# Performance work log

Measured on AMD Instinct MI355X. Metric: run time of the kernel, lower is better.

The kernel has to match this reference:

```python
import jax, jax.numpy as jnp
import numpy as np

N, D, H, B = 8192, 1024, 100, 32  # pairs, key dim, MLP hidden, batch_size


def setup_inputs() -> dict:
    key = jax.random.key(0)
    ks = jax.random.split(key, 6)
    q = jax.random.normal(ks[0], (N, D), jnp.float32)
    x = jax.random.normal(ks[1], (N, D), jnp.float32)
    b = jax.random.randint(ks[2], (N,), 0, B, dtype=jnp.int32)
    y = jax.random.randint(ks[3], (N,), 0, 2, dtype=jnp.int32)
    # Encoder params: Linear(2D -> H), ReLU, Linear(H -> 1)
    W1 = jax.random.normal(ks[4], (2 * D, H), jnp.float32) * (1.0 / np.sqrt(2 * D))
    b1 = jnp.zeros((H,), jnp.float32)
    W2 = jax.random.normal(ks[5], (H, 1), jnp.float32) * (1.0 / np.sqrt(H))
    b2 = jnp.zeros((1,), jnp.float32)
    return {"b": b, "q": q, "x": x, "y": y, "W1": W1, "b1": b1, "W2": W2, "b2": b2}


def reference(b, q, x, y, W1, b1, W2, b2):
    # Encoder: score per (query, key) pair
    inp = jnp.concatenate([q, x], axis=1)              # (N, 2D)
    h = jax.nn.relu(inp @ W1 + b1)                     # (N, H)
    s = (h @ W2 + b2)[:, 0]                            # (N,)

    n = s.shape[0]
    r = jnp.arange(n)
    yb = y.astype(bool)
    # pair mask: same batch element, differing labels, upper triangle
    m = (b[:, None] == b[None, :]) \
        & (yb[:, None] ^ yb[None, :]) \
        & (r[:, None] < r[None, :])                    # (N, N) bool

    d = s[:, None] - s[None, :]                        # (N, N) score diffs (logits)
    z = y.astype(jnp.float32)[:, None]                 # row label broadcast as target
    # stable BCE-with-logits, masked mean (== BCEWithLogitsLoss over selected pairs)
    bce = jnp.maximum(d, 0.0) - d * z + jnp.log1p(jnp.exp(-jnp.abs(d)))
    mf = m.astype(jnp.float32)
    loss = jnp.sum(bce * mf) / jnp.sum(mf)
    return loss
```

## Files before the change

### kernel.cpp

```cpp
#include <hip/hip_runtime.h>
#include <math.h>
#include <stdint.h>

#define NN 8192
#define DD 1024
#define KT 2048
#define HH 100
#define HP 128
#define LCAP 512
#define NB 32
#define NCH 16

typedef short bf16x8 __attribute__((ext_vector_type(8)));
typedef short bf16x4 __attribute__((ext_vector_type(4)));
typedef float f32x4 __attribute__((ext_vector_type(4)));

__device__ __forceinline__ short f2bf(float f) {
    uint32_t u = __builtin_bit_cast(uint32_t, f);
    u += 0x7FFF + ((u >> 16) & 1);
    return (short)(u >> 16);
}

__global__ __launch_bounds__(256) void prep_w1p(const float* __restrict__ W1,
                                                short* __restrict__ w1p,
                                                int* __restrict__ cnt1,
                                                int* __restrict__ cnt0)
{
    __shared__ float ld[32][104];
    const int t  = threadIdx.x;
    if (blockIdx.x == 0 && t < 64) {
        if (t < 32) cnt1[t] = 0; else cnt0[t - 32] = 0;
    }
    const int k0 = blockIdx.x * 32;
    for (int i = t; i < 32 * HH; i += 256) {
        const int kk = i / HH, cc = i - kk * HH;
        ld[kk][cc] = W1[(size_t)(k0 + kk) * HH + cc];
    }
    __syncthreads();
    for (int idx = t; idx < 512; idx += 256) {
        const int tt = idx >> 6, l = idx & 63;
        const int lr = l & 15, lg = l >> 4;
        const int col = tt * 16 + lr;
        bf16x8 r;
#pragma unroll
        for (int j = 0; j < 8; ++j)
            r[j] = (col < HH) ? f2bf(ld[lg * 8 + j][col]) : (short)0;
        *(bf16x8*)(w1p + ((size_t)(blockIdx.x * 8 + tt) * 64 + l) * 8) = r;
    }
}

__global__ __launch_bounds__(512) void encoder_mfma(
    const float* __restrict__ q, const float* __restrict__ x,
    const short* __restrict__ w1p,
    const float* __restrict__ b1, const float* __restrict__ W2,
    const float* __restrict__ b2,
    const int* __restrict__ bidx, const int* __restrict__ y,
    float* __restrict__ sp, float* __restrict__ sn,
    int* __restrict__ cnt1, int* __restrict__ cnt0)
{
    __shared__ short As[2][16][NCH][64];
    __shared__ float hsum[16][HP + 4];
    __shared__ float fold[4][16];
    const int t    = threadIdx.x;
    const int w    = t >> 6;
    const int half = w >> 2;
    const int wc   = w & 3;
    const int l    = t & 63;
    const int lr   = l & 15;
    const int lg   = l >> 4;
    const int r0   = blockIdx.x * 16;

    const int ts    = t & 255;
    const int srow  = ts >> 4;
    const int sslot = ts & 15;
    const int wslot = (sslot ^ srow) * 4;
    const float* abase = (half ? x : q) + (size_t)(r0 + srow) * DD + sslot * 4;
    auto cvt4 = [&](const float4& v) {
        bf16x4 s;
        s[0] = f2bf(v.x); s[1] = f2bf(v.y); s[2] = f2bf(v.z); s[3] = f2bf(v.w);
        return s;
    };
    {
        float4 g[8];
#pragma unroll
        for (int p = 0; p < 8; ++p) g[p] = *(const float4*)(abase + p * 64);
#pragma unroll
        for (int p = 0; p < 8; ++p)
            *(bf16x4*)&As[half][srow][p][wslot] = cvt4(g[p]);
#pragma unroll
        for (int p = 0; p < 8; ++p) g[p] = *(const float4*)(abase + (p + 8) * 64);
#pragma unroll
        for (int p = 0; p < 8; ++p)
            *(bf16x4*)&As[half][srow][p + 8][wslot] = cvt4(g[p]);
    }
    __syncthreads();

    const int p0 = ((2 * lg)     ^ lr) * 4;
    const int p1 = ((2 * lg + 1) ^ lr) * 4;
    const int p2 = ((2 * lg + 8) ^ lr) * 4;
    const int p3 = ((2 * lg + 9) ^ lr) * 4;

    const short* pB = w1p + (size_t)half * NCH * 8192
                    + ((size_t)(2 * wc) * 64 + l) * 8;
#define LOADB(c, x0, x1, x2, x3)                           \
    { const size_t e_ = (size_t)(c) * 8192;                \
      x0 = *(const bf16x8*)(pB + e_);                      \
      x1 = *(const bf16x8*)(pB + e_ + 4096);               \
      x2 = *(const bf16x8*)(pB + e_ + 512);                \
      x3 = *(const bf16x8*)(pB + e_ + 4096 + 512); }

    f32x4 acc0 = (f32x4)0.f, acc1 = (f32x4)0.f;
    bf16x8 bA0, bA1, bA2, bA3, bB0, bB1, bB2, bB3;

#define FRAGS_MFMA(c, b0, b1_, b2_, b3_)                                    \
    { const short* ar = &As[half][lr][c][0];                                \
      bf16x4 g0 = *(const bf16x4*)(ar + p0);                                \
      bf16x4 g1 = *(const bf16x4*)(ar + p1);                                \
      bf16x4 g2 = *(const bf16x4*)(ar + p2);                                \
      bf16x4 g3 = *(const bf16x4*)(ar + p3);                                \
      bf16x8 aa0 = __builtin_shufflevector(g0, g1, 0,1,2,3,4,5,6,7);        \
      bf16x8 aa1 = __builtin_shufflevector(g2, g3, 0,1,2,3,4,5,6,7);        \
      acc0 = __builtin_amdgcn_mfma_f32_16x16x32_bf16(aa0, b0,  acc0, 0,0,0);\
      acc0 = __builtin_amdgcn_mfma_f32_16x16x32_bf16(aa1, b1_, acc0, 0,0,0);\
      acc1 = __builtin_amdgcn_mfma_f32_16x16x32_bf16(aa0, b2_, acc1, 0,0,0);\
      acc1 = __builtin_amdgcn_mfma_f32_16x16x32_bf16(aa1, b3_, acc1, 0,0,0); }

    LOADB(0, bA0, bA1, bA2, bA3);
#pragma unroll 2
    for (int c = 0; c < NCH; c += 2) {
        LOADB(c + 1, bB0, bB1, bB2, bB3);
        FRAGS_MFMA(c, bA0, bA1, bA2, bA3);
        { const int cn = (c + 2 < NCH) ? c + 2 : 0; LOADB(cn, bA0, bA1, bA2, bA3); }
        FRAGS_MFMA(c + 1, bB0, bB1, bB2, bB3);
    }

    if (half == 0) {
#pragma unroll
        for (int r = 0; r < 4; ++r) {
            hsum[lg * 4 + r][wc * 32 + lr]      = acc0[r];
            hsum[lg * 4 + r][wc * 32 + lr + 16] = acc1[r];
        }
    }
    __syncthreads();
    if (half == 1) {
#pragma unroll
        for (int r = 0; r < 4; ++r) {
            hsum[lg * 4 + r][wc * 32 + lr]      += acc0[r];
            hsum[lg * 4 + r][wc * 32 + lr + 16] += acc1[r];
        }
    }
    __syncthreads();
    if (half == 0) {
        const int c0 = wc * 32 + lr;
        const int c1 = c0 + 16;
        const float bb0 = (c0 < HH) ? b1[c0] : 0.f;
        const float ww0 = (c0 < HH) ? W2[c0] : 0.f;
        const float bb1 = (c1 < HH) ? b1[c1] : 0.f;
        const float ww1 = (c1 < HH) ? W2[c1] : 0.f;
#pragma unroll
        for (int r = 0; r < 4; ++r) {
            const int row = lg * 4 + r;
            float v = fmaf(fmaxf(hsum[row][c0] + bb0, 0.f), ww0,
                           fmaxf(hsum[row][c1] + bb1, 0.f) * ww1);
            v += __shfl_xor(v, 1);
            v += __shfl_xor(v, 2);
            v += __shfl_xor(v, 4);
            v += __shfl_xor(v, 8);
            if (lr == 0) fold[wc][row] = v;
        }
    }
    __syncthreads();
    if (t < 16) {
        const float sv = fold[0][t] + fold[1][t] + fold[2][t] + fold[3][t] + b2[0];
        const int i = r0 + t;
        const int g = bidx[i];
        if (y[i]) {
            int idx = atomicAdd(&cnt1[g], 1);
            if (idx < LCAP) sp[g * LCAP + idx] = sv;
        } else {
            int idx = atomicAdd(&cnt0[g], 1);
            if (idx < LCAP) sn[g * LCAP + idx] = sv;
        }
    }
#undef LOADB
#undef FRAGS_MFMA
}

__global__ __launch_bounds__(256) void pairsum_kernel(
    const float* __restrict__ sp, const float* __restrict__ sn,
    const int* __restrict__ cnt1, const int* __restrict__ cnt0,
    float* __restrict__ partial)
{
    __shared__ float lsn[LCAP];
    __shared__ float lsp[64];
    __shared__ float wsum[4];
    const int g  = blockIdx.x >> 3;
    const int sl = blockIdx.x & 7;
    const int t  = threadIdx.x;
    const int n1 = min(cnt1[g], LCAP);
    const int n0 = min(cnt0[g], LCAP);
    for (int j = t; j < n0; j += 256) lsn[j] = sn[g * LCAP + j];
    const int np = (n1 > sl) ? ((n1 - sl + 7) >> 3) : 0;
    for (int j = t; j < np; j += 256) lsp[j] = sp[g * LCAP + sl + j * 8];
    __syncthreads();
    float acc = 0.f;
    const int total = np * n0;
    for (int u = t; u < total; u += 256) {
        const int ip = u / n0;
        const int j  = u - ip * n0;
        const float d  = lsn[j] - lsp[ip];
        const float ad = fabsf(d);
        const float z  = __builtin_exp2f(-ad * 1.44269504f);
        acc += fmaxf(d, 0.f) + __builtin_log2f(1.f + z) * 0.69314718f;
    }
#pragma unroll
    for (int off = 32; off > 0; off >>= 1) acc += __shfl_xor(acc, off, 64);
    const int wid = t >> 6, lane = t & 63;
    if (lane == 0) wsum[wid] = acc;
    __syncthreads();
    if (t == 0) partial[blockIdx.x] = wsum[0] + wsum[1] + wsum[2] + wsum[3];
}

__global__ __launch_bounds__(256) void finalize_kernel(
    const float* __restrict__ partial,
    const int* __restrict__ cnt1, const int* __restrict__ cnt0,
    float* __restrict__ out)
{
    __shared__ float ws_[4], wc_[4];
    const int t = threadIdx.x;
    float sv = partial[t];
    float cv = 0.f;
    if (t < NB) cv = (float)min(cnt1[t], LCAP) * (float)min(cnt0[t], LCAP);
#pragma unroll
    for (int off = 32; off > 0; off >>= 1) {
        sv += __shfl_xor(sv, off, 64);
        cv += __shfl_xor(cv, off, 64);
    }
    const int wid = t >> 6, lane = t & 63;
    if (lane == 0) { ws_[wid] = sv; wc_[wid] = cv; }
    __syncthreads();
    if (t == 0)
        out[0] = (ws_[0] + ws_[1] + ws_[2] + ws_[3]) /
                 (wc_[0] + wc_[1] + wc_[2] + wc_[3]);
}

extern "C" void kernel_launch(void* const* d_in, const int* in_sizes, int n_in,
                              void* d_out, int out_size, void* d_ws, size_t ws_size,
                              hipStream_t stream)
{
    const int*   b  = (const int*)d_in[0];
    const float* q  = (const float*)d_in[1];
    const float* x  = (const float*)d_in[2];
    const int*   y  = (const int*)d_in[3];
    const float* W1 = (const float*)d_in[4];
    const float* b1 = (const float*)d_in[5];
    const float* W2 = (const float*)d_in[6];
    const float* b2 = (const float*)d_in[7];
    float* out = (float*)d_out;

    char* base = (char*)d_ws;
    short* w1p     = (short*)base;
    float* sp      = (float*)(base + 524288);
    float* sn      = (float*)(base + 524288 + 65536);
    int*   cnt1    = (int*)(base + 524288 + 131072);
    int*   cnt0    = cnt1 + NB;
    float* partial = (float*)(base + 524288 + 131072 + 256);

    prep_w1p<<<KT / 32, 256, 0, stream>>>(W1, w1p, cnt1, cnt0);
    encoder_mfma<<<NN / 16, 512, 0, stream>>>(q, x, w1p, b1, W2, b2,
                                              b, y, sp, sn, cnt1, cnt0);
    pairsum_kernel<<<NB * 8, 256, 0, stream>>>(sp, sn, cnt1, cnt0, partial);
    finalize_kernel<<<1, 256, 0, stream>>>(partial, cnt1, cnt0, out);
}
```

Measured before the change: 51.74 us.

## Process 32 rows per block with full-K waves, staging q then x sequentially

The encoder block now covers 32 rows instead of 16. Each of the 8 waves owns 16 hidden columns over the full K dimension, instead of splitting K into q/x halves and reducing through shared memory. Each W1 fragment is reused for two 16-row MFMA tiles, which halves W1 global traffic per row and removes the hsum cross-wave reduction. The cost is that staging of the q half and the x half is serialised with extra barriers and no overlap. It also launches only 256 blocks, which may underfill the GPU.

```diff
diff --git a/kernel.cpp b/kernel.cpp
--- a/kernel.cpp
+++ b/kernel.cpp
@@ -6,10 +6,8 @@
 #define DD 1024
 #define KT 2048
 #define HH 100
-#define HP 128
 #define LCAP 512
 #define NB 32
-#define NCH 16
 
 typedef short bf16x8 __attribute__((ext_vector_type(8)));
 typedef short bf16x4 __attribute__((ext_vector_type(4)));
@@ -58,120 +56,115 @@
     float* __restrict__ sp, float* __restrict__ sn,
     int* __restrict__ cnt1, int* __restrict__ cnt0)
 {
-    __shared__ short As[2][16][NCH][64];
-    __shared__ float hsum[16][HP + 4];
-    __shared__ float fold[4][16];
-    const int t    = threadIdx.x;
-    const int w    = t >> 6;
-    const int half = w >> 2;
-    const int wc   = w & 3;
-    const int l    = t & 63;
-    const int lr   = l & 15;
-    const int lg   = l >> 4;
-    const int r0   = blockIdx.x * 16;
-
-    const int ts    = t & 255;
-    const int srow  = ts >> 4;
-    const int sslot = ts & 15;
-    const int wslot = (sslot ^ srow) * 4;
-    const float* abase = (half ? x : q) + (size_t)(r0 + srow) * DD + sslot * 4;
-    auto cvt4 = [&](const float4& v) {
-        bf16x4 s;
-        s[0] = f2bf(v.x); s[1] = f2bf(v.y); s[2] = f2bf(v.z); s[3] = f2bf(v.w);
-        return s;
+    __shared__ short As[32][16][64];
+    __shared__ float fold[8][32];
+    const int t  = threadIdx.x;
+    const int w  = t >> 6;
+    const int l  = t & 63;
+    const int lr = l & 15;
+    const int lg = l >> 4;
+    const int r0 = blockIdx.x * 32;
+
+    const int srow  = t >> 4;
+    const int sslot = t & 15;
+    const int wslot = (sslot ^ (srow & 15)) * 4;
+    auto stageHalf = [&](const float* base) {
+        const float* ab = base + (size_t)(r0 + srow) * DD + sslot * 4;
+        float4 g[8];
+#pragma unroll
+        for (int j = 0; j < 8; ++j) g[j] = *(const float4*)(ab + j * 64);
+#pragma unroll
+        for (int j = 0; j < 8; ++j) {
+            bf16x4 s;
+            s[0]=f2bf(g[j].x); s[1]=f2bf(g[j].y); s[2]=f2bf(g[j].z); s[3]=f2bf(g[j].w);
+            *(bf16x4*)&As[srow][j][wslot] = s;
+        }
+#pragma unroll
+        for (int j = 0; j < 8; ++j) g[j] = *(const float4*)(ab + (j + 8) * 64);
+#pragma unroll
+        for (int j = 0; j < 8; ++j) {
+            bf16x4 s;
+            s[0]=f2bf(g[j].x); s[1]=f2bf(g[j].y); s[2]=f2bf(g[j].z); s[3]=f2bf(g[j].w);
+            *(bf16x4*)&As[srow][j + 8][wslot] = s;
+        }
     };
-    {
-        float4 g[8];
-#pragma unroll
-        for (int p = 0; p < 8; ++p) g[p] = *(const float4*)(abase + p * 64);
-#pragma unroll
-        for (int p = 0; p < 8; ++p)
-            *(bf16x4*)&As[half][srow][p][wslot] = cvt4(g[p]);
-#pragma unroll
-        for (int p = 0; p < 8; ++p) g[p] = *(const float4*)(abase + (p + 8) * 64);
-#pragma unroll
-        for (int p = 0; p < 8; ++p)
-            *(bf16x4*)&As[half][srow][p + 8][wslot] = cvt4(g[p]);
-    }
-    __syncthreads();
 
     const int p0 = ((2 * lg)     ^ lr) * 4;
     const int p1 = ((2 * lg + 1) ^ lr) * 4;
     const int p2 = ((2 * lg + 8) ^ lr) * 4;
     const int p3 = ((2 * lg + 9) ^ lr) * 4;
 
-    const short* pB = w1p + (size_t)half * NCH * 8192
-                    + ((size_t)(2 * wc) * 64 + l) * 8;
-#define LOADB(c, x0, x1, x2, x3)                           \
-    { const size_t e_ = (size_t)(c) * 8192;                \
-      x0 = *(const bf16x8*)(pB + e_);                      \
-      x1 = *(const bf16x8*)(pB + e_ + 4096);               \
-      x2 = *(const bf16x8*)(pB + e_ + 512);                \
-      x3 = *(const bf16x8*)(pB + e_ + 4096 + 512); }
-
+    const short* pB = w1p + (size_t)w * 512 + (size_t)l * 8;
     f32x4 acc0 = (f32x4)0.f, acc1 = (f32x4)0.f;
-    bf16x8 bA0, bA1, bA2, bA3, bB0, bB1, bB2, bB3;
-
-#define FRAGS_MFMA(c, b0, b1_, b2_, b3_)                                    \
-    { const short* ar = &As[half][lr][c][0];                                \
-      bf16x4 g0 = *(const bf16x4*)(ar + p0);                                \
-      bf16x4 g1 = *(const bf16x4*)(ar + p1);                                \
-      bf16x4 g2 = *(const bf16x4*)(ar + p2);                                \
-      bf16x4 g3 = *(const bf16x4*)(ar + p3);                                \
+    bf16x8 bA0, bA1, bB0, bB1;
+
+#define LOADB2(h, c, b0, b1_)                                        \
+    { const size_t e_ = ((size_t)(h) * 32 + 2 * (c)) * 4096;         \
+      b0  = *(const bf16x8*)(pB + e_);                               \
+      b1_ = *(const bf16x8*)(pB + e_ + 4096); }
+
+#define FRAGS(c, b0, b1_)                                                   \
+    { const short* a0 = &As[lr][c][0];                                      \
+      const short* a1 = &As[lr + 16][c][0];                                 \
+      bf16x4 g0 = *(const bf16x4*)(a0 + p0);                                \
+      bf16x4 g1 = *(const bf16x4*)(a0 + p1);                                \
+      bf16x4 g2 = *(const bf16x4*)(a0 + p2);                                \
+      bf16x4 g3 = *(const bf16x4*)(a0 + p3);                                \
+      bf16x4 h0 = *(const bf16x4*)(a1 + p0);                                \
+      bf16x4 h1 = *(const bf16x4*)(a1 + p1);                                \
+      bf16x4 h2 = *(const bf16x4*)(a1 + p2);                                \
+      bf16x4 h3 = *(const bf16x4*)(a1 + p3);                                \
       bf16x8 aa0 = __builtin_shufflevector(g0, g1, 0,1,2,3,4,5,6,7);        \
       bf16x8 aa1 = __builtin_shufflevector(g2, g3, 0,1,2,3,4,5,6,7);        \
+      bf16x8 cc0 = __builtin_shufflevector(h0, h1, 0,1,2,3,4,5,6,7);        \
+      bf16x8 cc1 = __builtin_shufflevector(h2, h3, 0,1,2,3,4,5,6,7);        \
       acc0 = __builtin_amdgcn_mfma_f32_16x16x32_bf16(aa0, b0,  acc0, 0,0,0);\
       acc0 = __builtin_amdgcn_mfma_f32_16x16x32_bf16(aa1, b1_, acc0, 0,0,0);\
-      acc1 = __builtin_amdgcn_mfma_f32_16x16x32_bf16(aa0, b2_, acc1, 0,0,0);\
-      acc1 = __builtin_amdgcn_mfma_f32_16x16x32_bf16(aa1, b3_, acc1, 0,0,0); }
-
-    LOADB(0, bA0, bA1, bA2, bA3);
-#pragma unroll 2
-    for (int c = 0; c < NCH; c += 2) {
-        LOADB(c + 1, bB0, bB1, bB2, bB3);
-        FRAGS_MFMA(c, bA0, bA1, bA2, bA3);
-        { const int cn = (c + 2 < NCH) ? c + 2 : 0; LOADB(cn, bA0, bA1, bA2, bA3); }
-        FRAGS_MFMA(c + 1, bB0, bB1, bB2, bB3);
-    }
-
-    if (half == 0) {
-#pragma unroll
-        for (int r = 0; r < 4; ++r) {
-            hsum[lg * 4 + r][wc * 32 + lr]      = acc0[r];
-            hsum[lg * 4 + r][wc * 32 + lr + 16] = acc1[r];
-        }
-    }
-    __syncthreads();
-    if (half == 1) {
-#pragma unroll
-        for (int r = 0; r < 4; ++r) {
-            hsum[lg * 4 + r][wc * 32 + lr]      += acc0[r];
-            hsum[lg * 4 + r][wc * 32 + lr + 16] += acc1[r];
-        }
-    }
-    __syncthreads();
-    if (half == 0) {
-        const int c0 = wc * 32 + lr;
-        const int c1 = c0 + 16;
-        const float bb0 = (c0 < HH) ? b1[c0] : 0.f;
-        const float ww0 = (c0 < HH) ? W2[c0] : 0.f;
-        const float bb1 = (c1 < HH) ? b1[c1] : 0.f;
-        const float ww1 = (c1 < HH) ? W2[c1] : 0.f;
-#pragma unroll
-        for (int r = 0; r < 4; ++r) {
-            const int row = lg * 4 + r;
-            float v = fmaf(fmaxf(hsum[row][c0] + bb0, 0.f), ww0,
-                           fmaxf(hsum[row][c1] + bb1, 0.f) * ww1);
-            v += __shfl_xor(v, 1);
-            v += __shfl_xor(v, 2);
-            v += __shfl_xor(v, 4);
-            v += __shfl_xor(v, 8);
-            if (lr == 0) fold[wc][row] = v;
-        }
-    }
-    __syncthreads();
-    if (t < 16) {
-        const float sv = fold[0][t] + fold[1][t] + fold[2][t] + fold[3][t] + b2[0];
+      acc1 = __builtin_amdgcn_mfma_f32_16x16x32_bf16(cc0, b0,  acc1, 0,0,0);\
+      acc1 = __builtin_amdgcn_mfma_f32_16x16x32_bf16(cc1, b1_, acc1, 0,0,0); }
+
+#define COMPUTE_HALF(h)                                              \
+    { LOADB2(h, 0, bA0, bA1)                                         \
+      _Pragma("unroll 1")                                            \
+      for (int c = 0; c < 16; c += 2) {                              \
+          LOADB2(h, c + 1, bB0, bB1)                                 \
+          FRAGS(c, bA0, bA1)                                         \
+          if (c + 2 < 16) { LOADB2(h, c + 2, bA0, bA1) }             \
+          FRAGS(c + 1, bB0, bB1)                                     \
+      } }
+
+    stageHalf(q);
+    __syncthreads();
+    COMPUTE_HALF(0)
+    __syncthreads();
+    stageHalf(x);
+    __syncthreads();
+    COMPUTE_HALF(1)
+#undef LOADB2
+#undef FRAGS
+#undef COMPUTE_HALF
+
+    const int col = w * 16 + lr;
+    const float bb = (col < HH) ? b1[col] : 0.f;
+    const float ww = (col < HH) ? W2[col] : 0.f;
+#pragma unroll
+    for (int r = 0; r < 4; ++r) {
+        float v0 = fmaxf(acc0[r] + bb, 0.f) * ww;
+        float v1 = fmaxf(acc1[r] + bb, 0.f) * ww;
+        v0 += __shfl_xor(v0, 1); v1 += __shfl_xor(v1, 1);
+        v0 += __shfl_xor(v0, 2); v1 += __shfl_xor(v1, 2);
+        v0 += __shfl_xor(v0, 4); v1 += __shfl_xor(v1, 4);
+        v0 += __shfl_xor(v0, 8); v1 += __shfl_xor(v1, 8);
+        if (lr == 0) {
+            fold[w][lg * 4 + r]      = v0;
+            fold[w][16 + lg * 4 + r] = v1;
+        }
+    }
+    __syncthreads();
+    if (t < 32) {
+        float sv = b2[0];
+#pragma unroll
+        for (int ws_ = 0; ws_ < 8; ++ws_) sv += fold[ws_][t];
         const int i = r0 + t;
         const int g = bidx[i];
         if (y[i]) {
@@ -182,8 +175,6 @@
             if (idx < LCAP) sn[g * LCAP + idx] = sv;
         }
     }
-#undef LOADB
-#undef FRAGS_MFMA
 }
 
 __global__ __launch_bounds__(256) void pairsum_kernel(
@@ -267,7 +258,7 @@
     float* partial = (float*)(base + 524288 + 131072 + 256);
 
     prep_w1p<<<KT / 32, 256, 0, stream>>>(W1, w1p, cnt1, cnt0);
-    encoder_mfma<<<NN / 16, 512, 0, stream>>>(q, x, w1p, b1, W2, b2,
+    encoder_mfma<<<NN / 32, 512, 0, stream>>>(q, x, w1p, b1, W2, b2,
                                               b, y, sp, sn, cnt1, cnt0);
     pairsum_kernel<<<NB * 8, 256, 0, stream>>>(sp, sn, cnt1, cnt0, partial);
     finalize_kernel<<<1, 256, 0, stream>>>(partial, cnt1, cnt0, out);
```

Result: no change. 51.19 us (-1.0%).
